# Kernel tuning notes

Hardware: AMD Instinct MI355X
Metric: run time of the kernel (lower is better)

The kernel has to match this reference:

```python
import jax, jax.numpy as jnp
import numpy as np

B_, H_, W_, C_ = 8, 56, 56, 96
D_ = int(C_ * 2.0)          # d_inner = 192
N_ = 16                     # d_state
K_ = 4                      # scan directions
R_ = (C_ + 15) // 16        # dt_rank 'auto' = 6
MLP_H = 4 * C_
EPS = 1e-5


def setup_inputs() -> dict:
    key = jax.random.key(0)
    ks = jax.random.split(key, 16)
    s = 0.02
    rn = lambda k, sh, sc=1.0: jax.random.normal(k, sh, dtype=jnp.float32) * sc
    return dict(
        x=rn(ks[0], (B_, H_, W_, C_)),
        ln1_w=jnp.ones((C_,), jnp.float32), ln1_b=jnp.zeros((C_,), jnp.float32),
        in_proj_w=rn(ks[1], (2 * D_, C_), s),
        conv_w=rn(ks[2], (D_, 1, 3, 3), s), conv_b=jnp.zeros((D_,), jnp.float32),
        x_proj_w=rn(ks[3], (K_, R_ + 2 * N_, D_), s),
        dt_proj_w=rn(ks[4], (K_, D_, R_), s),
        dt_proj_b=rn(ks[5], (K_, D_), 0.1),
        A_logs=jax.random.uniform(ks[6], (K_ * D_, N_), jnp.float32, 0.0, 3.0),
        Ds=jnp.ones((K_ * D_,), jnp.float32),
        out_norm_w=jnp.ones((D_,), jnp.float32), out_norm_b=jnp.zeros((D_,), jnp.float32),
        out_proj_w=rn(ks[7], (C_, D_), s),
        ln2_w=jnp.ones((C_,), jnp.float32), ln2_b=jnp.zeros((C_,), jnp.float32),
        fc1_w=rn(ks[8], (MLP_H, C_), s), fc1_b=jnp.zeros((MLP_H,), jnp.float32),
        fc2_w=rn(ks[9], (C_, MLP_H), s), fc2_b=jnp.zeros((C_,), jnp.float32),
    )


def layer_norm(x, w, b):
    m = x.mean(-1, keepdims=True)
    v = ((x - m) ** 2).mean(-1, keepdims=True)
    return (x - m) / jnp.sqrt(v + EPS) * w + b


def ss2d(x, in_proj_w, conv_w, conv_b, x_proj_w, dt_proj_w, dt_proj_b,
         A_logs, Ds, out_norm_w, out_norm_b, out_proj_w):
    Bn, Hh, Ww, C = x.shape
    L = Hh * Ww
    xz = x @ in_proj_w.T                       # (B,H,W,2D)
    xc, z = jnp.split(xz, 2, axis=-1)
    xc = xc.transpose(0, 3, 1, 2)              # (B,D,H,W)
    xc = jax.lax.conv_general_dilated(xc, conv_w, (1, 1), 'SAME',
                                      feature_group_count=D_)
    xc = jax.nn.silu(xc + conv_b[None, :, None, None])
    # cross-scan: 4 traversal orders, each (B,D,L)
    x0 = xc.reshape(Bn, D_, L)
    x1 = xc.transpose(0, 1, 3, 2).reshape(Bn, D_, L)
    xs = jnp.stack([x0, x1, x0[..., ::-1], x1[..., ::-1]], axis=1)  # (B,K,D,L)
    xdbl = jnp.einsum('bkdl,kcd->bkcl', xs, x_proj_w)
    dts, Bs, Cs = jnp.split(xdbl, [R_, R_ + N_], axis=2)            # (B,K,R,L),(B,K,N,L)x2
    dts = jnp.einsum('bkrl,kdr->bkdl', dts, dt_proj_w)
    dts = jax.nn.softplus(dts + dt_proj_b[None, :, :, None])        # (B,K,D,L)
    A = -jnp.exp(A_logs).reshape(K_, D_, N_)                        # (K,D,N)

    def step(h, inp):
        xt, dtt, Bt, Ct = inp                  # (B,K,D),(B,K,D),(B,K,N),(B,K,N)
        h = h * jnp.exp(dtt[..., None] * A) + (dtt * xt)[..., None] * Bt[:, :, None, :]
        return h, jnp.einsum('bkdn,bkn->bkd', h, Ct)

    inps = (xs.transpose(3, 0, 1, 2), dts.transpose(3, 0, 1, 2),
            Bs.transpose(3, 0, 1, 2), Cs.transpose(3, 0, 1, 2))
    h0 = jnp.zeros((Bn, K_, D_, N_), jnp.float32)
    _, ys = jax.lax.scan(step, h0, inps)       # (L,B,K,D)
    ys = ys.transpose(1, 2, 3, 0)              # (B,K,D,L)
    ys = ys + Ds.reshape(K_, D_)[None, :, :, None] * xs
    # cross-merge: undo flips and transposed order
    y = ys[:, 0] + ys[:, 2, :, ::-1]
    y = y + (ys[:, 1] + ys[:, 3, :, ::-1]).reshape(Bn, D_, Ww, Hh) \
            .transpose(0, 1, 3, 2).reshape(Bn, D_, L)
    y = y.transpose(0, 2, 1).reshape(Bn, Hh, Ww, D_)
    y = layer_norm(y, out_norm_w, out_norm_b)
    y = y * jax.nn.silu(z)
    return y @ out_proj_w.T


def reference(x, ln1_w, ln1_b, in_proj_w, conv_w, conv_b, x_proj_w, dt_proj_w,
              dt_proj_b, A_logs, Ds, out_norm_w, out_norm_b, out_proj_w,
              ln2_w, ln2_b, fc1_w, fc1_b, fc2_w, fc2_b):
    # norm -> SS2D -> residual
    x = x + ss2d(layer_norm(x, ln1_w, ln1_b), in_proj_w, conv_w, conv_b,
                 x_proj_w, dt_proj_w, dt_proj_b, A_logs, Ds,
                 out_norm_w, out_norm_b, out_proj_w)
    # norm -> MLP -> residual
    h = layer_norm(x, ln2_w, ln2_b)
    h = jax.nn.gelu(h @ fc1_w.T + fc1_b) @ fc2_w.T + fc2_b
    return x + h
```

## Files before the change

kernel.cpp:

```cpp
#include <hip/hip_runtime.h>
#include <hip/hip_bf16.h>

typedef __hip_bfloat16 bf16;
typedef short bf16x8 __attribute__((ext_vector_type(8)));
typedef float f32x4 __attribute__((ext_vector_type(4)));

#define BBATCH 8
#define HHH 56
#define WWW 56
#define CCH 96
#define DIN 192
#define NST 16
#define KDIR 4
#define RDT 6
#define LLEN 3136
#define BLTOT 25088
#define SSEG 64
#define SEGL 49
#define PJC 38
#define PJW 152
#define PJS 40
#define PJS1 24
#define MLPH 384

__device__ __forceinline__ float b2f(bf16 v) { return __bfloat162float(v); }
__device__ __forceinline__ bf16  f2b(float v) { return __float2bfloat16(v); }
__device__ __forceinline__ unsigned short f2bu(float f) {
    union { bf16 h; unsigned short u; } c; c.h = __float2bfloat16(f); return c.u;
}
__device__ __forceinline__ float sigm(float x) { return 1.f / (1.f + __expf(-x)); }
__device__ __forceinline__ float softplusf(float x) {
    return fmaxf(x, 0.f) + __logf(1.f + __expf(-fabsf(x)));
}
__device__ __forceinline__ float geluf(float v) {
    float u = 0.7978845608028654f * (v + 0.044715f * v * v * v);
    float ey = __expf(2.f * u);
    float th = 1.f - 2.f / (ey + 1.f);
    return 0.5f * v * (1.f + th);
}

__device__ __forceinline__ int pos_map(int k, int l) {
    if (k & 2) l = LLEN - 1 - l;
    if (k & 1) { int q = l / WWW; int r = l - q * WWW; return r * WWW + q; }
    return l;
}

__global__ __launch_bounds__(256) void ln_rows(
    const float* __restrict__ xin, const float* __restrict__ w,
    const float* __restrict__ b, unsigned short* __restrict__ xn) {
    int row = blockIdx.x * 4 + (threadIdx.x >> 6);
    int lane = threadIdx.x & 63;
    const float* xr = xin + (size_t)row * 96;
    float2 v = make_float2(0.f, 0.f);
    if (lane < 48) v = *(const float2*)&xr[lane * 2];
    float s = v.x + v.y, s2 = v.x * v.x + v.y * v.y;
    for (int o = 32; o; o >>= 1) {
        s += __shfl_down(s, o);
        s2 += __shfl_down(s2, o);
    }
    s = __shfl(s, 0); s2 = __shfl(s2, 0);
    float m = s * (1.f / 96.f);
    float var = s2 * (1.f / 96.f) - m * m;
    float rs = rsqrtf(var + 1e-5f);
    if (lane < 48) {
        float o0 = (v.x - m) * rs * w[lane * 2] + b[lane * 2];
        float o1 = (v.y - m) * rs * w[lane * 2 + 1] + b[lane * 2 + 1];
        ushort2 u; u.x = f2bu(o0); u.y = f2bu(o1);
        *(ushort2*)&xn[(size_t)row * 96 + lane * 2] = u;
    }
}

template<int N, int K, int EPI>
__global__ __launch_bounds__(256) void gemm_mfma(
    const unsigned short* __restrict__ X, const float* __restrict__ W,
    const float* __restrict__ bias, const float* __restrict__ res,
    void* __restrict__ out0v, void* __restrict__ out1v) {
    __shared__ unsigned short a_sh[256 * 40];
    __shared__ unsigned short b_sh[64 * 40];
    const int t = threadIdx.x;
    const int P0 = blockIdx.x * 256;
    const int N0 = blockIdx.y * 64;
    const int w = t >> 6, lane = t & 63, q = lane >> 4, nl = lane & 15;
    f32x4 acc[4][4];
#pragma unroll
    for (int i = 0; i < 4; ++i)
#pragma unroll
        for (int j = 0; j < 4; ++j)
            acc[i][j] = (f32x4){0.f, 0.f, 0.f, 0.f};
    for (int k0 = 0; k0 < K; k0 += 32) {
        __syncthreads();
#pragma unroll
        for (int it = 0; it < 4; ++it) {
            int idx = t + it * 256;
            int pr = idx >> 2, kq = idx & 3;
            uint4 v = *(const uint4*)&X[(size_t)(P0 + pr) * K + k0 + kq * 8];
            *(uint4*)&a_sh[pr * 40 + kq * 8] = v;
        }
#pragma unroll
        for (int it = 0; it < 2; ++it) {
            int idx = t + it * 256;
            int nr = idx >> 3, kq = idx & 7;
            int ng = N0 + nr; if (ng > N - 1) ng = N - 1;
            float4 v = *(const float4*)&W[(size_t)ng * K + k0 + kq * 4];
            ushort4 u;
            u.x = f2bu(v.x); u.y = f2bu(v.y); u.z = f2bu(v.z); u.w = f2bu(v.w);
            *(ushort4*)&b_sh[nr * 40 + kq * 4] = u;
        }
        __syncthreads();
        bf16x8 af[4], bfr[4];
#pragma unroll
        for (int mf = 0; mf < 4; ++mf)
            af[mf] = *(const bf16x8*)&a_sh[(w * 64 + mf * 16 + nl) * 40 + q * 8];
#pragma unroll
        for (int nf = 0; nf < 4; ++nf)
            bfr[nf] = *(const bf16x8*)&b_sh[(nf * 16 + nl) * 40 + q * 8];
#pragma unroll
        for (int mf = 0; mf < 4; ++mf)
#pragma unroll
            for (int nf = 0; nf < 4; ++nf)
                acc[mf][nf] = __builtin_amdgcn_mfma_f32_16x16x32_bf16(
                    af[mf], bfr[nf], acc[mf][nf], 0, 0, 0);
    }
#pragma unroll
    for (int mf = 0; mf < 4; ++mf) {
#pragma unroll
        for (int nf = 0; nf < 4; ++nf) {
#pragma unroll
            for (int r = 0; r < 4; ++r) {
                float v = acc[mf][nf][r];
                size_t pos = (size_t)P0 + w * 64 + mf * 16 + q * 4 + r;
                int n = N0 + nf * 16 + nl;
                if constexpr (EPI == 0) {
                    unsigned short* xc = (unsigned short*)out0v;
                    unsigned short* zz = (unsigned short*)out1v;
                    if (n < 192) xc[pos * 192 + n] = f2bu(v);
                    else         zz[pos * 192 + (n - 192)] = f2bu(v);
                } else if constexpr (EPI == 1) {
                    if (n < 152) ((float*)out0v)[pos * 152 + n] = v;
                } else if constexpr (EPI == 2) {
                    if (n < 96) ((float*)out0v)[pos * 96 + n] = res[pos * 96 + n] + v;
                } else if constexpr (EPI == 3) {
                    ((unsigned short*)out0v)[pos * 384 + n] = f2bu(geluf(v + bias[n]));
                } else {
                    if (n < 96) ((float*)out0v)[pos * 96 + n] =
                        res[pos * 96 + n] + bias[n] + v;
                }
            }
        }
    }
}

__global__ __launch_bounds__(256) void k2_conv(
    const bf16* __restrict__ xcpre, const float* __restrict__ cw,
    const float* __restrict__ cb, bf16* __restrict__ xconv) {
    int idx = blockIdx.x * 256 + threadIdx.x;
    int d = idx % DIN;
    int P = idx / DIN;
    int b = P / LLEN, l = P - b * LLEN;
    int h = l / WWW, w = l - h * WWW;
    float acc = cb[d];
#pragma unroll
    for (int i = 0; i < 3; ++i) {
        int hh = h + i - 1;
        if (hh < 0 || hh >= HHH) continue;
#pragma unroll
        for (int j = 0; j < 3; ++j) {
            int ww = w + j - 1;
            if (ww < 0 || ww >= WWW) continue;
            float xv = b2f(xcpre[((size_t)(b * LLEN + hh * WWW + ww)) * DIN + d]);
            acc = fmaf(xv, cw[d * 9 + i * 3 + j], acc);
        }
    }
    acc = acc * sigm(acc);
    xconv[(size_t)P * DIN + d] = f2b(acc);
}

__global__ __launch_bounds__(192) void k4_scan1(
    const bf16* __restrict__ xconv, const float* __restrict__ proj,
    const float* __restrict__ dtw, const float* __restrict__ dtb,
    const float* __restrict__ Alog, float* __restrict__ hloc,
    float* __restrict__ tsum) {
    __shared__ float pl[SEGL * PJS1];
    __shared__ int posl[SEGL];
    const int bid = blockIdx.x;
    const int s = bid & 63, k = (bid >> 6) & 3, b = bid >> 8;
    const int d = threadIdx.x;
    const int l0 = s * SEGL;
    for (int q = d; q < SEGL * 22; q += 192) {
        int st = q / 22, c = q - st * 22;
        int p = pos_map(k, l0 + st);
        int ofs = (c < 6) ? c : c + 2;
        pl[st * PJS1 + ofs] = proj[(size_t)(b * LLEN + p) * PJW + k * PJC + c];
    }
    if (d < SEGL) posl[d] = pos_map(k, l0 + d) * DIN;
    float w6[RDT];
#pragma unroll
    for (int r = 0; r < RDT; ++r) w6[r] = dtw[(k * DIN + d) * RDT + r];
    const float bias = dtb[k * DIN + d];
    float a[NST];
#pragma unroll
    for (int n = 0; n < NST; ++n) a[n] = -__expf(Alog[(k * DIN + d) * NST + n]);
    float h[NST];
#pragma unroll
    for (int n = 0; n < NST; ++n) h[n] = 0.f;
    float T = 0.f;
    __syncthreads();
    const bf16* xg = xconv + (size_t)b * LLEN * DIN + d;
    for (int bt = 0; bt < 7; ++bt) {
        int off7[7]; float xv7[7];
#pragma unroll
        for (int i = 0; i < 7; ++i) off7[i] = posl[bt * 7 + i];
#pragma unroll
        for (int i = 0; i < 7; ++i) xv7[i] = b2f(xg[off7[i]]);
#pragma unroll
        for (int i = 0; i < 7; ++i) {
            const float* rowf = &pl[(bt * 7 + i) * PJS1];
            float4 g0 = *(const float4*)(rowf);
            float2 g1 = *(const float2*)(rowf + 4);
            float dtv = bias;
            dtv = fmaf(g0.x, w6[0], dtv); dtv = fmaf(g0.y, w6[1], dtv);
            dtv = fmaf(g0.z, w6[2], dtv); dtv = fmaf(g0.w, w6[3], dtv);
            dtv = fmaf(g1.x, w6[4], dtv); dtv = fmaf(g1.y, w6[5], dtv);
            dtv = softplusf(dtv);
            T += dtv;
            float u = dtv * xv7[i];
#pragma unroll
            for (int g = 0; g < 4; ++g) {
                float4 Bv = *(const float4*)(rowf + 8 + 4 * g);
                float e0 = __expf(dtv * a[4 * g + 0]);
                float e1 = __expf(dtv * a[4 * g + 1]);
                float e2 = __expf(dtv * a[4 * g + 2]);
                float e3 = __expf(dtv * a[4 * g + 3]);
                h[4 * g + 0] = fmaf(h[4 * g + 0], e0, u * Bv.x);
                h[4 * g + 1] = fmaf(h[4 * g + 1], e1, u * Bv.y);
                h[4 * g + 2] = fmaf(h[4 * g + 2], e2, u * Bv.z);
                h[4 * g + 3] = fmaf(h[4 * g + 3], e3, u * Bv.w);
            }
        }
    }
    size_t base = ((size_t)bid * DIN + d) * NST;
#pragma unroll
    for (int n = 0; n < NST; ++n) hloc[base + n] = h[n];
    tsum[bid * DIN + d] = T;
}

__global__ __launch_bounds__(256) void k5_carry(
    const float* hloc, const float* __restrict__ tsum,
    const float* __restrict__ Alog, float* hin) {
    int g = blockIdx.x * 256 + threadIdx.x;
    int n = g & 15;
    int dk = g >> 4;
    int d = dk % DIN;
    int bk = dk / DIN;
    int k = bk & 3;
    float a = -__expf(Alog[(k * DIN + d) * NST + n]);
    float Hc = 0.f;
    for (int s = 0; s < SSEG; ++s) {
        int bid = bk * SSEG + s;
        size_t idx = ((size_t)bid * DIN + d) * NST + n;
        float hl = hloc[idx];
        float Tv = tsum[bid * DIN + d];
        hin[idx] = Hc;
        Hc = fmaf(__expf(a * Tv), Hc, hl);
    }
}

__global__ __launch_bounds__(192) void k6_scan2(
    const bf16* __restrict__ xconv, const float* __restrict__ proj,
    const float* __restrict__ dtw, const float* __restrict__ dtb,
    const float* __restrict__ Alog, const float* __restrict__ Dsp,
    const float* __restrict__ hin, bf16* __restrict__ ysm) {
    __shared__ float pl[SEGL * PJS];
    __shared__ int posl[SEGL];
    const int bid = blockIdx.x;
    const int s = bid & 63, k = (bid >> 6) & 3, b = bid >> 8;
    const int d = threadIdx.x;
    const int l0 = s * SEGL;
    for (int q = d; q < SEGL * PJC; q += 192) {
        int st = q / PJC, c = q - st * PJC;
        int p = pos_map(k, l0 + st);
        int ofs = (c < 6) ? c : c + 2;
        pl[st * PJS + ofs] = proj[(size_t)(b * LLEN + p) * PJW + k * PJC + c];
    }
    if (d < SEGL) posl[d] = pos_map(k, l0 + d) * DIN;
    float w6[RDT];
#pragma unroll
    for (int r = 0; r < RDT; ++r) w6[r] = dtw[(k * DIN + d) * RDT + r];
    const float bias = dtb[k * DIN + d];
    const float dsv = Dsp[k * DIN + d];
    float a[NST];
#pragma unroll
    for (int n = 0; n < NST; ++n) a[n] = -__expf(Alog[(k * DIN + d) * NST + n]);
    float h[NST];
    size_t hbase = ((size_t)bid * DIN + d) * NST;
#pragma unroll
    for (int n = 0; n < NST; ++n) h[n] = hin[hbase + n];
    __syncthreads();
    const bf16* xg = xconv + (size_t)b * LLEN * DIN + d;
    bf16* ysg = ysm + ((size_t)(b * KDIR + k) * LLEN) * DIN + d;
    for (int bt = 0; bt < 7; ++bt) {
        int off7[7]; float xv7[7];
#pragma unroll
        for (int i = 0; i < 7; ++i) off7[i] = posl[bt * 7 + i];
#pragma unroll
        for (int i = 0; i < 7; ++i) xv7[i] = b2f(xg[off7[i]]);
#pragma unroll
        for (int i = 0; i < 7; ++i) {
            const float* rowf = &pl[(bt * 7 + i) * PJS];
            float4 g0 = *(const float4*)(rowf);
            float2 g1 = *(const float2*)(rowf + 4);
            float dtv = bias;
            dtv = fmaf(g0.x, w6[0], dtv); dtv = fmaf(g0.y, w6[1], dtv);
            dtv = fmaf(g0.z, w6[2], dtv); dtv = fmaf(g0.w, w6[3], dtv);
            dtv = fmaf(g1.x, w6[4], dtv); dtv = fmaf(g1.y, w6[5], dtv);
            dtv = softplusf(dtv);
            float u = dtv * xv7[i];
            float y = dsv * xv7[i];
#pragma unroll
            for (int g = 0; g < 4; ++g) {
                float4 Bv = *(const float4*)(rowf + 8 + 4 * g);
                float4 Cv = *(const float4*)(rowf + 24 + 4 * g);
                float e0 = __expf(dtv * a[4 * g + 0]);
                float e1 = __expf(dtv * a[4 * g + 1]);
                float e2 = __expf(dtv * a[4 * g + 2]);
                float e3 = __expf(dtv * a[4 * g + 3]);
                h[4 * g + 0] = fmaf(h[4 * g + 0], e0, u * Bv.x);
                h[4 * g + 1] = fmaf(h[4 * g + 1], e1, u * Bv.y);
                h[4 * g + 2] = fmaf(h[4 * g + 2], e2, u * Bv.z);
                h[4 * g + 3] = fmaf(h[4 * g + 3], e3, u * Bv.w);
                y = fmaf(h[4 * g + 0], Cv.x, y);
                y = fmaf(h[4 * g + 1], Cv.y, y);
                y = fmaf(h[4 * g + 2], Cv.z, y);
                y = fmaf(h[4 * g + 3], Cv.w, y);
            }
            ysg[off7[i]] = f2b(y);
        }
    }
}

__global__ __launch_bounds__(256) void k65_merge(
    const bf16* __restrict__ ysm, const bf16* __restrict__ z,
    const float* __restrict__ onw, const float* __restrict__ onb,
    bf16* __restrict__ ymod) {
    __shared__ float rb[16 * DIN];
    __shared__ float ps[256], pq[256];
    __shared__ float mrow[16], srow[16];
    const int t = threadIdx.x;
    const int P0 = blockIdx.x * 16;
    for (int q = t; q < 16 * DIN; q += 256) {
        int pos = q / DIN, c = q - pos * DIN;
        int P = P0 + pos;
        int b = P / LLEN, l = P - b * LLEN;
        size_t base = ((size_t)(b * KDIR) * LLEN + l) * DIN + c;
        size_t pstr = (size_t)LLEN * DIN;
        float v = b2f(ysm[base]) + b2f(ysm[base + pstr]) +
                  b2f(ysm[base + 2 * pstr]) + b2f(ysm[base + 3 * pstr]);
        rb[q] = v;
    }
    __syncthreads();
    {
        int pos = t >> 4, part = t & 15;
        float s = 0.f, s2 = 0.f;
        for (int i = 0; i < 12; ++i) {
            float v = rb[pos * DIN + part * 12 + i];
            s += v; s2 += v * v;
        }
        ps[pos * 16 + part] = s; pq[pos * 16 + part] = s2;
    }
    __syncthreads();
    if (t < 16) {
        float s = 0.f, s2 = 0.f;
        for (int i = 0; i < 16; ++i) { s += ps[t * 16 + i]; s2 += pq[t * 16 + i]; }
        float m = s * (1.f / DIN);
        float v = s2 * (1.f / DIN) - m * m;
        mrow[t] = m; srow[t] = rsqrtf(v + 1e-5f);
    }
    __syncthreads();
    for (int q = t; q < 16 * DIN; q += 256) {
        int pos = q / DIN, c = q - pos * DIN;
        int P = P0 + pos;
        float v = (rb[q] - mrow[pos]) * srow[pos] * onw[c] + onb[c];
        float zv = b2f(z[(size_t)P * DIN + c]);
        v *= zv * sigm(zv);
        ymod[(size_t)P * DIN + c] = f2b(v);
    }
}

extern "C" void kernel_launch(void* const* d_in, const int* in_sizes, int n_in,
                              void* d_out, int out_size, void* d_ws, size_t ws_size,
                              hipStream_t stream) {
    const float* x      = (const float*)d_in[0];
    const float* ln1w   = (const float*)d_in[1];
    const float* ln1b   = (const float*)d_in[2];
    const float* inpW   = (const float*)d_in[3];
    const float* convW  = (const float*)d_in[4];
    const float* convB  = (const float*)d_in[5];
    const float* xprojW = (const float*)d_in[6];
    const float* dtW    = (const float*)d_in[7];
    const float* dtB    = (const float*)d_in[8];
    const float* Alog   = (const float*)d_in[9];
    const float* Dsp    = (const float*)d_in[10];
    const float* onw    = (const float*)d_in[11];
    const float* onb    = (const float*)d_in[12];
    const float* outW   = (const float*)d_in[13];
    const float* ln2w   = (const float*)d_in[14];
    const float* ln2b   = (const float*)d_in[15];
    const float* fc1W   = (const float*)d_in[16];
    const float* fc1b   = (const float*)d_in[17];
    const float* fc2W   = (const float*)d_in[18];
    const float* fc2b   = (const float*)d_in[19];
    float* out = (float*)d_out;

    char* ws = (char*)d_ws;
    unsigned short* z_us    = (unsigned short*)(ws + 0);
    bf16*  z_bf             = (bf16*)z_us;
    bf16*  xconv_bf         = (bf16*)(ws + 9633792);
    float* proj_f           = (float*)(ws + 19267584);
    bf16*  ymod_bf          = (bf16*)(ws + 19267584);
    unsigned short* xn_us   = (unsigned short*)(ws + 34521088);
    float* tsum_f           = (float*)(ws + 34521088);
    unsigned short* xcpre_us= (unsigned short*)(ws + 39337984);
    bf16*  xcpre_bf         = (bf16*)xcpre_us;
    float* hloc_f           = (float*)(ws + 48971776);
    float* hin_f            = hloc_f;
    float* y1_f             = (float*)(ws + 48971776);
    unsigned short* y1n_us  = (unsigned short*)(ws + 58605568);
    bf16*  ysm_bf           = (bf16*)(ws + 74137600);
    unsigned short* hmlp_us = (unsigned short*)(ws + 74137600);

    ln_rows<<<6272, 256, 0, stream>>>(x, ln1w, ln1b, xn_us);
    gemm_mfma<384, 96, 0><<<dim3(98, 6), 256, 0, stream>>>(
        xn_us, inpW, nullptr, nullptr, xcpre_us, z_us);
    k2_conv<<<18816, 256, 0, stream>>>(xcpre_bf, convW, convB, xconv_bf);
    gemm_mfma<152, 192, 1><<<dim3(98, 3), 256, 0, stream>>>(
        (const unsigned short*)xconv_bf, xprojW, nullptr, nullptr, proj_f, nullptr);
    k4_scan1<<<2048, 192, 0, stream>>>(xconv_bf, proj_f, dtW, dtB, Alog, hloc_f, tsum_f);
    k5_carry<<<384, 256, 0, stream>>>(hloc_f, tsum_f, Alog, hin_f);
    k6_scan2<<<2048, 192, 0, stream>>>(xconv_bf, proj_f, dtW, dtB, Alog, Dsp, hin_f, ysm_bf);
    k65_merge<<<1568, 256, 0, stream>>>(ysm_bf, z_bf, onw, onb, ymod_bf);
    gemm_mfma<96, 192, 2><<<dim3(98, 2), 256, 0, stream>>>(
        (const unsigned short*)ymod_bf, outW, nullptr, x, y1_f, nullptr);
    ln_rows<<<6272, 256, 0, stream>>>(y1_f, ln2w, ln2b, y1n_us);
    gemm_mfma<384, 96, 3><<<dim3(98, 6), 256, 0, stream>>>(
        y1n_us, fc1W, fc1b, nullptr, hmlp_us, nullptr);
    gemm_mfma<96, 384, 4><<<dim3(98, 2), 256, 0, stream>>>(
        hmlp_us, fc2W, fc2b, y1_f, out, nullptr);
}
```

Baseline: 417.3 us.

## Interleave two scan segments per thread, use exp2 intrinsics, vectorize conv

Each scan block now handles two adjacent 49-step segments at once, interleaving two independent recurrences per thread to expose instruction-level parallelism and hide exp/FMA latency, with half as many blocks. The exponentials in the scans, carry and softplus are switched to native exp2/log2 builtins with a folded log2(e) factor, removing a multiply per exp. The depthwise conv processes two channels per thread with packed 32-bit loads and stores. The trade-offs are higher register pressure from two state vectors and fewer blocks available to fill the GPU.

```diff
diff --git a/kernel.cpp b/kernel.cpp
--- a/kernel.cpp
+++ b/kernel.cpp
@@ -23,6 +23,22 @@
 #define PJS1 24
 #define MLPH 384
 
+#if defined(__has_builtin)
+#if __has_builtin(__builtin_amdgcn_exp2f)
+#define EXP2F(x) __builtin_amdgcn_exp2f(x)
+#endif
+#if __has_builtin(__builtin_amdgcn_logf)
+#define LOG2F_(x) __builtin_amdgcn_logf(x)
+#endif
+#endif
+#ifndef EXP2F
+#define EXP2F(x) __expf((x) * 0.69314718056f)
+#endif
+#ifndef LOG2F_
+#define LOG2F_(x) (__logf(x) * 1.44269504f)
+#endif
+#define LOG2E 1.44269504f
+
 __device__ __forceinline__ float b2f(bf16 v) { return __bfloat162float(v); }
 __device__ __forceinline__ bf16  f2b(float v) { return __float2bfloat16(v); }
 __device__ __forceinline__ unsigned short f2bu(float f) {
@@ -30,7 +46,8 @@
 }
 __device__ __forceinline__ float sigm(float x) { return 1.f / (1.f + __expf(-x)); }
 __device__ __forceinline__ float softplusf(float x) {
-    return fmaxf(x, 0.f) + __logf(1.f + __expf(-fabsf(x)));
+    float t = EXP2F(-fabsf(x) * LOG2E);
+    return fmaxf(x, 0.f) + 0.69314718f * LOG2F_(1.f + t);
 }
 __device__ __forceinline__ float geluf(float v) {
     float u = 0.7978845608028654f * (v + 0.044715f * v * v * v);
@@ -151,14 +168,15 @@
 }
 
 __global__ __launch_bounds__(256) void k2_conv(
-    const bf16* __restrict__ xcpre, const float* __restrict__ cw,
-    const float* __restrict__ cb, bf16* __restrict__ xconv) {
+    const unsigned short* __restrict__ xcpre, const float* __restrict__ cw,
+    const float* __restrict__ cb, unsigned short* __restrict__ xconv) {
     int idx = blockIdx.x * 256 + threadIdx.x;
-    int d = idx % DIN;
-    int P = idx / DIN;
+    int dd = idx % 96;
+    int P = idx / 96;
+    int d0 = dd * 2;
     int b = P / LLEN, l = P - b * LLEN;
     int h = l / WWW, w = l - h * WWW;
-    float acc = cb[d];
+    float acc0 = cb[d0], acc1 = cb[d0 + 1];
 #pragma unroll
     for (int i = 0; i < 3; ++i) {
         int hh = h + i - 1;
@@ -167,12 +185,18 @@
         for (int j = 0; j < 3; ++j) {
             int ww = w + j - 1;
             if (ww < 0 || ww >= WWW) continue;
-            float xv = b2f(xcpre[((size_t)(b * LLEN + hh * WWW + ww)) * DIN + d]);
-            acc = fmaf(xv, cw[d * 9 + i * 3 + j], acc);
-        }
-    }
-    acc = acc * sigm(acc);
-    xconv[(size_t)P * DIN + d] = f2b(acc);
+            ushort2 xv = *(const ushort2*)&xcpre[
+                ((size_t)(b * LLEN + hh * WWW + ww)) * DIN + d0];
+            union { unsigned short u; bf16 h_; } c0, c1;
+            c0.u = xv.x; c1.u = xv.y;
+            acc0 = fmaf(b2f(c0.h_), cw[d0 * 9 + i * 3 + j], acc0);
+            acc1 = fmaf(b2f(c1.h_), cw[(d0 + 1) * 9 + i * 3 + j], acc1);
+        }
+    }
+    acc0 = acc0 * sigm(acc0);
+    acc1 = acc1 * sigm(acc1);
+    ushort2 o; o.x = f2bu(acc0); o.y = f2bu(acc1);
+    *(ushort2*)&xconv[(size_t)P * DIN + d0] = o;
 }
 
 __global__ __launch_bounds__(192) void k4_scan1(
@@ -180,68 +204,79 @@
     const float* __restrict__ dtw, const float* __restrict__ dtb,
     const float* __restrict__ Alog, float* __restrict__ hloc,
     float* __restrict__ tsum) {
-    __shared__ float pl[SEGL * PJS1];
-    __shared__ int posl[SEGL];
+    __shared__ float pl[98 * PJS1];
+    __shared__ int posl[98];
     const int bid = blockIdx.x;
-    const int s = bid & 63, k = (bid >> 6) & 3, b = bid >> 8;
+    const int s2 = bid & 31, k = (bid >> 5) & 3, b = bid >> 7;
     const int d = threadIdx.x;
-    const int l0 = s * SEGL;
-    for (int q = d; q < SEGL * 22; q += 192) {
+    const int l0 = s2 * (2 * SEGL);
+    for (int q = d; q < 98 * 22; q += 192) {
         int st = q / 22, c = q - st * 22;
         int p = pos_map(k, l0 + st);
         int ofs = (c < 6) ? c : c + 2;
         pl[st * PJS1 + ofs] = proj[(size_t)(b * LLEN + p) * PJW + k * PJC + c];
     }
-    if (d < SEGL) posl[d] = pos_map(k, l0 + d) * DIN;
+    if (d < 98) posl[d] = pos_map(k, l0 + d) * DIN;
     float w6[RDT];
 #pragma unroll
     for (int r = 0; r < RDT; ++r) w6[r] = dtw[(k * DIN + d) * RDT + r];
     const float bias = dtb[k * DIN + d];
-    float a[NST];
-#pragma unroll
-    for (int n = 0; n < NST; ++n) a[n] = -__expf(Alog[(k * DIN + d) * NST + n]);
-    float h[NST];
-#pragma unroll
-    for (int n = 0; n < NST; ++n) h[n] = 0.f;
-    float T = 0.f;
+    float a2[NST];
+#pragma unroll
+    for (int n = 0; n < NST; ++n)
+        a2[n] = -__expf(Alog[(k * DIN + d) * NST + n]) * LOG2E;
+    float hA[NST], hB[NST];
+#pragma unroll
+    for (int n = 0; n < NST; ++n) { hA[n] = 0.f; hB[n] = 0.f; }
+    float TA = 0.f, TB = 0.f;
     __syncthreads();
     const bf16* xg = xconv + (size_t)b * LLEN * DIN + d;
     for (int bt = 0; bt < 7; ++bt) {
-        int off7[7]; float xv7[7];
-#pragma unroll
-        for (int i = 0; i < 7; ++i) off7[i] = posl[bt * 7 + i];
-#pragma unroll
-        for (int i = 0; i < 7; ++i) xv7[i] = b2f(xg[off7[i]]);
+        int offA[7], offB[7]; float xvA[7], xvB[7];
+#pragma unroll
+        for (int i = 0; i < 7; ++i) { offA[i] = posl[bt * 7 + i]; offB[i] = posl[49 + bt * 7 + i]; }
+#pragma unroll
+        for (int i = 0; i < 7; ++i) { xvA[i] = b2f(xg[offA[i]]); xvB[i] = b2f(xg[offB[i]]); }
 #pragma unroll
         for (int i = 0; i < 7; ++i) {
-            const float* rowf = &pl[(bt * 7 + i) * PJS1];
-            float4 g0 = *(const float4*)(rowf);
-            float2 g1 = *(const float2*)(rowf + 4);
-            float dtv = bias;
-            dtv = fmaf(g0.x, w6[0], dtv); dtv = fmaf(g0.y, w6[1], dtv);
-            dtv = fmaf(g0.z, w6[2], dtv); dtv = fmaf(g0.w, w6[3], dtv);
-            dtv = fmaf(g1.x, w6[4], dtv); dtv = fmaf(g1.y, w6[5], dtv);
-            dtv = softplusf(dtv);
-            T += dtv;
-            float u = dtv * xv7[i];
+            const float* rA = &pl[(bt * 7 + i) * PJS1];
+            const float* rB = &pl[(49 + bt * 7 + i) * PJS1];
+            float4 gA0 = *(const float4*)(rA); float2 gA1 = *(const float2*)(rA + 4);
+            float4 gB0 = *(const float4*)(rB); float2 gB1 = *(const float2*)(rB + 4);
+            float dA = bias, dB = bias;
+            dA = fmaf(gA0.x, w6[0], dA); dB = fmaf(gB0.x, w6[0], dB);
+            dA = fmaf(gA0.y, w6[1], dA); dB = fmaf(gB0.y, w6[1], dB);
+            dA = fmaf(gA0.z, w6[2], dA); dB = fmaf(gB0.z, w6[2], dB);
+            dA = fmaf(gA0.w, w6[3], dA); dB = fmaf(gB0.w, w6[3], dB);
+            dA = fmaf(gA1.x, w6[4], dA); dB = fmaf(gB1.x, w6[4], dB);
+            dA = fmaf(gA1.y, w6[5], dA); dB = fmaf(gB1.y, w6[5], dB);
+            dA = softplusf(dA); dB = softplusf(dB);
+            TA += dA; TB += dB;
+            float uA = dA * xvA[i], uB = dB * xvB[i];
 #pragma unroll
             for (int g = 0; g < 4; ++g) {
-                float4 Bv = *(const float4*)(rowf + 8 + 4 * g);
-                float e0 = __expf(dtv * a[4 * g + 0]);
-                float e1 = __expf(dtv * a[4 * g + 1]);
-                float e2 = __expf(dtv * a[4 * g + 2]);
-                float e3 = __expf(dtv * a[4 * g + 3]);
-                h[4 * g + 0] = fmaf(h[4 * g + 0], e0, u * Bv.x);
-                h[4 * g + 1] = fmaf(h[4 * g + 1], e1, u * Bv.y);
-                h[4 * g + 2] = fmaf(h[4 * g + 2], e2, u * Bv.z);
-                h[4 * g + 3] = fmaf(h[4 * g + 3], e3, u * Bv.w);
+                float4 BA = *(const float4*)(rA + 8 + 4 * g);
+                float4 BB = *(const float4*)(rB + 8 + 4 * g);
+#pragma unroll
+                for (int m = 0; m < 4; ++m) {
+                    int n = 4 * g + m;
+                    float Bae = (m == 0) ? BA.x : (m == 1) ? BA.y : (m == 2) ? BA.z : BA.w;
+                    float Bbe = (m == 0) ? BB.x : (m == 1) ? BB.y : (m == 2) ? BB.z : BB.w;
+                    float eA = EXP2F(dA * a2[n]);
+                    float eB = EXP2F(dB * a2[n]);
+                    hA[n] = fmaf(hA[n], eA, uA * Bae);
+                    hB[n] = fmaf(hB[n], eB, uB * Bbe);
+                }
             }
         }
     }
-    size_t base = ((size_t)bid * DIN + d) * NST;
-#pragma unroll
-    for (int n = 0; n < NST; ++n) hloc[base + n] = h[n];
-    tsum[bid * DIN + d] = T;
+    const int bk = b * KDIR + k;
+    size_t baseA = ((size_t)(bk * SSEG + 2 * s2) * DIN + d) * NST;
+    size_t baseB = ((size_t)(bk * SSEG + 2 * s2 + 1) * DIN + d) * NST;
+#pragma unroll
+    for (int n = 0; n < NST; ++n) { hloc[baseA + n] = hA[n]; hloc[baseB + n] = hB[n]; }
+    tsum[(bk * SSEG + 2 * s2) * DIN + d] = TA;
+    tsum[(bk * SSEG + 2 * s2 + 1) * DIN + d] = TB;
 }
 
 __global__ __launch_bounds__(256) void k5_carry(
@@ -253,7 +288,7 @@
     int d = dk % DIN;
     int bk = dk / DIN;
     int k = bk & 3;
-    float a = -__expf(Alog[(k * DIN + d) * NST + n]);
+    float a2 = -__expf(Alog[(k * DIN + d) * NST + n]) * LOG2E;
     float Hc = 0.f;
     for (int s = 0; s < SSEG; ++s) {
         int bid = bk * SSEG + s;
@@ -261,7 +296,7 @@
         float hl = hloc[idx];
         float Tv = tsum[bid * DIN + d];
         hin[idx] = Hc;
-        Hc = fmaf(__expf(a * Tv), Hc, hl);
+        Hc = fmaf(EXP2F(a2 * Tv), Hc, hl);
     }
 }
 
@@ -270,70 +305,82 @@
     const float* __restrict__ dtw, const float* __restrict__ dtb,
     const float* __restrict__ Alog, const float* __restrict__ Dsp,
     const float* __restrict__ hin, bf16* __restrict__ ysm) {
-    __shared__ float pl[SEGL * PJS];
-    __shared__ int posl[SEGL];
+    __shared__ float pl[98 * PJS];
+    __shared__ int posl[98];
     const int bid = blockIdx.x;
-    const int s = bid & 63, k = (bid >> 6) & 3, b = bid >> 8;
+    const int s2 = bid & 31, k = (bid >> 5) & 3, b = bid >> 7;
     const int d = threadIdx.x;
-    const int l0 = s * SEGL;
-    for (int q = d; q < SEGL * PJC; q += 192) {
+    const int l0 = s2 * (2 * SEGL);
+    for (int q = d; q < 98 * PJC; q += 192) {
         int st = q / PJC, c = q - st * PJC;
         int p = pos_map(k, l0 + st);
         int ofs = (c < 6) ? c : c + 2;
         pl[st * PJS + ofs] = proj[(size_t)(b * LLEN + p) * PJW + k * PJC + c];
     }
-    if (d < SEGL) posl[d] = pos_map(k, l0 + d) * DIN;
+    if (d < 98) posl[d] = pos_map(k, l0 + d) * DIN;
     float w6[RDT];
 #pragma unroll
     for (int r = 0; r < RDT; ++r) w6[r] = dtw[(k * DIN + d) * RDT + r];
     const float bias = dtb[k * DIN + d];
     const float dsv = Dsp[k * DIN + d];
-    float a[NST];
-#pragma unroll
-    for (int n = 0; n < NST; ++n) a[n] = -__expf(Alog[(k * DIN + d) * NST + n]);
-    float h[NST];
-    size_t hbase = ((size_t)bid * DIN + d) * NST;
-#pragma unroll
-    for (int n = 0; n < NST; ++n) h[n] = hin[hbase + n];
+    float a2[NST];
+#pragma unroll
+    for (int n = 0; n < NST; ++n)
+        a2[n] = -__expf(Alog[(k * DIN + d) * NST + n]) * LOG2E;
+    const int bk = b * KDIR + k;
+    float hA[NST], hB[NST];
+    size_t hbA = ((size_t)(bk * SSEG + 2 * s2) * DIN + d) * NST;
+    size_t hbB = ((size_t)(bk * SSEG + 2 * s2 + 1) * DIN + d) * NST;
+#pragma unroll
+    for (int n = 0; n < NST; ++n) { hA[n] = hin[hbA + n]; hB[n] = hin[hbB + n]; }
     __syncthreads();
     const bf16* xg = xconv + (size_t)b * LLEN * DIN + d;
-    bf16* ysg = ysm + ((size_t)(b * KDIR + k) * LLEN) * DIN + d;
+    bf16* ysg = ysm + ((size_t)bk * LLEN) * DIN + d;
     for (int bt = 0; bt < 7; ++bt) {
-        int off7[7]; float xv7[7];
-#pragma unroll
-        for (int i = 0; i < 7; ++i) off7[i] = posl[bt * 7 + i];
-#pragma unroll
-        for (int i = 0; i < 7; ++i) xv7[i] = b2f(xg[off7[i]]);
+        int offA[7], offB[7]; float xvA[7], xvB[7];
+#pragma unroll
+        for (int i = 0; i < 7; ++i) { offA[i] = posl[bt * 7 + i]; offB[i] = posl[49 + bt * 7 + i]; }
+#pragma unroll
+        for (int i = 0; i < 7; ++i) { xvA[i] = b2f(xg[offA[i]]); xvB[i] = b2f(xg[offB[i]]); }
 #pragma unroll
         for (int i = 0; i < 7; ++i) {
-            const float* rowf = &pl[(bt * 7 + i) * PJS];
-            float4 g0 = *(const float4*)(rowf);
-            float2 g1 = *(const float2*)(rowf + 4);
-            float dtv = bias;
-            dtv = fmaf(g0.x, w6[0], dtv); dtv = fmaf(g0.y, w6[1], dtv);
-            dtv = fmaf(g0.z, w6[2], dtv); dtv = fmaf(g0.w, w6[3], dtv);
-            dtv = fmaf(g1.x, w6[4], dtv); dtv = fmaf(g1.y, w6[5], dtv);
-            dtv = softplusf(dtv);
-            float u = dtv * xv7[i];
-            float y = dsv * xv7[i];
+            const float* rA = &pl[(bt * 7 + i) * PJS];
+            const float* rB = &pl[(49 + bt * 7 + i) * PJS];
+            float4 gA0 = *(const float4*)(rA); float2 gA1 = *(const float2*)(rA + 4);
+            float4 gB0 = *(const float4*)(rB); float2 gB1 = *(const float2*)(rB + 4);
+            float dA = bias, dB = bias;
+            dA = fmaf(gA0.x, w6[0], dA); dB = fmaf(gB0.x, w6[0], dB);
+            dA = fmaf(gA0.y, w6[1], dA); dB = fmaf(gB0.y, w6[1], dB);
+            dA = fmaf(gA0.z, w6[2], dA); dB = fmaf(gB0.z, w6[2], dB);
+            dA = fmaf(gA0.w, w6[3], dA); dB = fmaf(gB0.w, w6[3], dB);
+            dA = fmaf(gA1.x, w6[4], dA); dB = fmaf(gB1.x, w6[4], dB);
+            dA = fmaf(gA1.y, w6[5], dA); dB = fmaf(gB1.y, w6[5], dB);
+            dA = softplusf(dA); dB = softplusf(dB);
+            float uA = dA * xvA[i], uB = dB * xvB[i];
+            float yA = dsv * xvA[i], yB = dsv * xvB[i];
 #pragma unroll
             for (int g = 0; g < 4; ++g) {
-                float4 Bv = *(const float4*)(rowf + 8 + 4 * g);
-                float4 Cv = *(const float4*)(rowf + 24 + 4 * g);
-                float e0 = __expf(dtv * a[4 * g + 0]);
-                float e1 = __expf(dtv * a[4 * g + 1]);
-                float e2 = __expf(dtv * a[4 * g + 2]);
-                float e3 = __expf(dtv * a[4 * g + 3]);
-                h[4 * g + 0] = fmaf(h[4 * g + 0], e0, u * Bv.x);
-                h[4 * g + 1] = fmaf(h[4 * g + 1], e1, u * Bv.y);
-                h[4 * g + 2] = fmaf(h[4 * g + 2], e2, u * Bv.z);
-                h[4 * g + 3] = fmaf(h[4 * g + 3], e3, u * Bv.w);
-                y = fmaf(h[4 * g + 0], Cv.x, y);
-                y = fmaf(h[4 * g + 1], Cv.y, y);
-                y = fmaf(h[4 * g + 2], Cv.z, y);
-                y = fmaf(h[4 * g + 3], Cv.w, y);
+                float4 BA = *(const float4*)(rA + 8 + 4 * g);
+                float4 CA = *(const float4*)(rA + 24 + 4 * g);
+                float4 BB = *(const float4*)(rB + 8 + 4 * g);
+                float4 CB = *(const float4*)(rB + 24 + 4 * g);
+#pragma unroll
+                for (int m = 0; m < 4; ++m) {
+                    int n = 4 * g + m;
+                    float Bae = (m == 0) ? BA.x : (m == 1) ? BA.y : (m == 2) ? BA.z : BA.w;
+                    float Cae = (m == 0) ? CA.x : (m == 1) ? CA.y : (m == 2) ? CA.z : CA.w;
+                    float Bbe = (m == 0) ? BB.x : (m == 1) ? BB.y : (m == 2) ? BB.z : BB.w;
+                    float Cbe = (m == 0) ? CB.x : (m == 1) ? CB.y : (m == 2) ? CB.z : CB.w;
+                    float eA = EXP2F(dA * a2[n]);
+                    float eB = EXP2F(dB * a2[n]);
+                    hA[n] = fmaf(hA[n], eA, uA * Bae);
+                    hB[n] = fmaf(hB[n], eB, uB * Bbe);
+                    yA = fmaf(hA[n], Cae, yA);
+                    yB = fmaf(hB[n], Cbe, yB);
+                }
             }
-            ysg[off7[i]] = f2b(y);
+            ysg[offA[i]] = f2b(yA);
+            ysg[offB[i]] = f2b(yB);
         }
     }
 }
@@ -420,7 +467,6 @@
     unsigned short* xn_us   = (unsigned short*)(ws + 34521088);
     float* tsum_f           = (float*)(ws + 34521088);
     unsigned short* xcpre_us= (unsigned short*)(ws + 39337984);
-    bf16*  xcpre_bf         = (bf16*)xcpre_us;
     float* hloc_f           = (float*)(ws + 48971776);
     float* hin_f            = hloc_f;
     float* y1_f             = (float*)(ws + 48971776);
@@ -431,12 +477,13 @@
     ln_rows<<<6272, 256, 0, stream>>>(x, ln1w, ln1b, xn_us);
     gemm_mfma<384, 96, 0><<<dim3(98, 6), 256, 0, stream>>>(
         xn_us, inpW, nullptr, nullptr, xcpre_us, z_us);
-    k2_conv<<<18816, 256, 0, stream>>>(xcpre_bf, convW, convB, xconv_bf);
+    k2_conv<<<9408, 256, 0, stream>>>(xcpre_us, convW, convB,
+                                      (unsigned short*)xconv_bf);
     gemm_mfma<152, 192, 1><<<dim3(98, 3), 256, 0, stream>>>(
         (const unsigned short*)xconv_bf, xprojW, nullptr, nullptr, proj_f, nullptr);
-    k4_scan1<<<2048, 192, 0, stream>>>(xconv_bf, proj_f, dtW, dtB, Alog, hloc_f, tsum_f);
+    k4_scan1<<<1024, 192, 0, stream>>>(xconv_bf, proj_f, dtW, dtB, Alog, hloc_f, tsum_f);
     k5_carry<<<384, 256, 0, stream>>>(hloc_f, tsum_f, Alog, hin_f);
-    k6_scan2<<<2048, 192, 0, stream>>>(xconv_bf, proj_f, dtW, dtB, Alog, Dsp, hin_f, ysm_bf);
+    k6_scan2<<<1024, 192, 0, stream>>>(xconv_bf, proj_f, dtW, dtB, Alog, Dsp, hin_f, ysm_bf);
     k65_merge<<<1568, 256, 0, stream>>>(ysm_bf, z_bf, onw, onb, ymod_bf);
     gemm_mfma<96, 192, 2><<<dim3(98, 2), 256, 0, stream>>>(
         (const unsigned short*)ymod_bf, outW, nullptr, x, y1_f, nullptr);
```

After: 438.5 us. +5.1%, slower.
